# Optimization experiments

Measured on AMD Instinct MI355X. Metric: run time of the kernel, lower is better.

Reference implementation:

```python
import jax, jax.numpy as jnp
import numpy as np

C = 8           # feat_channel
B, N = 8, 64    # batch, max objects
H, W = 128, 128
D = (C + 2) * C + C + C * C + C + C + 1  # 169


def setup_inputs() -> dict:
    key = jax.random.key(0)
    k1, k2, k3, k4 = jax.random.split(key, 4)
    seg_feat = jax.random.normal(k1, (B, C, H, W), dtype=jnp.float32)
    conv_weight = jax.random.normal(k2, (B, D, H, W), dtype=jnp.float32)
    mask = jnp.ones((B, N), dtype=jnp.float32)
    ind = jax.random.randint(k3, (B, N), 0, H * W, dtype=jnp.int64)
    target = jax.random.uniform(k4, (B, N, H, W), dtype=jnp.float32)
    return {"seg_feat": seg_feat, "conv_weight": conv_weight, "mask": mask,
            "ind": ind, "target": target}


def reference(seg_feat, conv_weight, mask, ind, target):
    b, c, h, w = seg_feat.shape
    n = ind.shape[1]
    # _tranpose_and_gather_feat: [B,D,H,W] -> [B,HW,D] -> gather at ind -> [B,N,D]
    wflat = conv_weight.reshape(b, -1, h * w).transpose(0, 2, 1)
    weight = jnp.take_along_axis(wflat, ind[:, :, None], axis=1)  # [B,N,D]
    splits = np.cumsum([(c + 2) * c, c, c * c, c, c])
    w1, b1, w2, b2, w3, b3 = jnp.split(weight, splits, axis=-1)
    w1 = w1.reshape(b, n, c, c + 2)   # per-object conv1 1x1 weights
    w2 = w2.reshape(b, n, c, c)
    w3 = w3.reshape(b, n, 1, c)
    # object centers and relative coordinate maps
    x0 = (ind % w).astype(jnp.float32)
    y0 = (ind // w).astype(jnp.float32)
    xg = jnp.arange(w, dtype=jnp.float32)
    yg = jnp.arange(h, dtype=jnp.float32)
    y_grid, x_grid = jnp.meshgrid(yg, xg, indexing="ij")  # [H,W]
    x_rel = (x_grid[None, None] - x0[:, :, None, None]) / 128.0  # [B,N,H,W]
    y_rel = (y_grid[None, None] - y0[:, :, None, None]) / 128.0
    feat = jnp.concatenate(
        [jnp.broadcast_to(seg_feat[:, None], (b, n, c, h, w)),
         x_rel[:, :, None], y_rel[:, :, None]], axis=2)  # [B,N,C+2,H,W]
    # three grouped 1x1 convs == per-object channel contractions
    h1 = jax.nn.relu(jnp.einsum("bnoc,bnchw->bnohw", w1, feat) + b1[..., None, None])
    h2 = jax.nn.relu(jnp.einsum("bnoc,bnchw->bnohw", w2, h1) + b2[..., None, None])
    out = jax.nn.sigmoid(jnp.einsum("bnoc,bnchw->bnohw", w3, h2) + b3[..., None, None])[:, :, 0]  # [B,N,H,W]
    m = mask[:, :, None, None]
    pred = out * m
    tgt = target * m
    smooth = 1.0
    inter = jnp.sum(pred * tgt, axis=(1, 2, 3))
    denom = jnp.sum(pred * pred, axis=(1, 2, 3)) + jnp.sum(tgt * tgt, axis=(1, 2, 3))
    loss = 1.0 - (2.0 * inter + smooth) / (denom + smooth)  # per-image dice
    return jnp.mean(loss)  # sum over batch / batch_size
```

## Files before the change

### kernel.cpp

```cpp
#include <hip/hip_runtime.h>

#define Cc 8
#define Hh 128
#define Ww 128
#define Nn 64
#define Bb 8
#define Dd 169
#define HW (Hh * Ww)
#define NP 4
#define NPG 8
#define PXS 1024
#define NSTRIPE (HW / PXS)
#define NBLK (Bb * NPG * NSTRIPE)
#define FRAGW 16
#define FRAG_U32 (256 * 64 * FRAGW)
#define SLOTS (NPG * NSTRIPE)

#define INV128 (1.0f / 128.0f)

typedef __fp16 f16x2 __attribute__((ext_vector_type(2)));
typedef _Float16 h8 __attribute__((ext_vector_type(8)));
typedef float f32x4 __attribute__((ext_vector_type(4)));

static __device__ __forceinline__ uint32_t pku(float a, float b) {
    f16x2 t = __builtin_amdgcn_cvt_pkrtz(a, b);
    uint32_t u; __builtin_memcpy(&u, &t, 4); return u;
}
static __device__ __forceinline__ h8 u4h8(uint32_t a, uint32_t b, uint32_t c, uint32_t d) {
    uint32_t u[4] = {a, b, c, d}; h8 r; __builtin_memcpy(&r, u, 16); return r;
}

__global__ void pack_frags(const float* __restrict__ conv_weight,
                           const float* __restrict__ mask,
                           const int*   __restrict__ ind,
                           uint32_t*    __restrict__ frag) {
    const int npair = blockIdx.x;
    const int b     = npair >> 5;
    const int bn0   = b * Nn + 2 * (npair & 31);
    const int l  = threadIdx.x;
    const int g  = l >> 4, r = l & 15, rr = r & 7;
    const int bnr = bn0 + (r >> 3);
    const int bng = bn0 + (g >> 1);
    const float* base = conv_weight + (size_t)b * Dd * HW;
    const float* srcR = base + ind[bnr];
    const float* srcG = base + ind[bng];

    float a1[8];
    #pragma unroll
    for (int e = 0; e < 8; ++e) {
        const int k = 8 * g + e;
        float v = 0.f;
        if (k < 8)       v = srcR[(size_t)(rr * 10 + k) * HW];
        else if (k == 8) v = srcR[(size_t)(rr * 10 + 8) * HW];
        else if (k == 9) v = srcR[(size_t)(rr * 10 + 9) * HW];
        else if (k == 10) {
            const float w8 = srcR[(size_t)(rr * 10 + 8) * HW];
            const float w9 = srcR[(size_t)(rr * 10 + 9) * HW];
            const float b1 = srcR[(size_t)(80 + rr) * HW];
            const int   ib = ind[bnr];
            v = b1 - w8 * ((float)(ib & 127) * INV128)
                   - w9 * ((float)(ib >> 7) * INV128);
        }
        a1[e] = v;
    }
    float a2[4];
    #pragma unroll
    for (int e = 0; e < 4; ++e) {
        const int k2 = 4 * g + e;
        float v = 0.f;
        if (r < 8)  { if (k2 < 8)  v = srcR[(size_t)(88 + rr * 8 + k2) * HW]; }
        else        { if (k2 >= 8) v = srcR[(size_t)(88 + rr * 8 + (k2 - 8)) * HW]; }
        a2[e] = v;
    }
    const float b2bias = (g == 0) ? srcR[(size_t)(152 + rr) * HW] : 0.f;

    float w3v[4];
    #pragma unroll
    for (int j = 0; j < 4; ++j) {
        const int c = (4 * g + j) & 7;
        w3v[j] = srcG[(size_t)(160 + c) * HW];
    }
    const float b3 = srcG[(size_t)168 * HW];
    const float mm = mask[bng];

    uint32_t* dst = frag + ((size_t)npair * 64 + l) * FRAGW;
    dst[0] = pku(a1[0], a1[1]); dst[1] = pku(a1[2], a1[3]);
    dst[2] = pku(a1[4], a1[5]); dst[3] = pku(a1[6], a1[7]);
    dst[4] = pku(a2[0], a2[1]); dst[5] = pku(a2[2], a2[3]);
    dst[6] = pku(b2bias, 0.f);
    float* df = (float*)dst;
    df[7] = w3v[0]; df[8] = w3v[1]; df[9] = w3v[2]; df[10] = w3v[3];
    df[11] = b3; df[12] = mm * mm;
    dst[13] = 0u; dst[14] = 0u; dst[15] = 0u;
}

__global__ __launch_bounds__(256)
__attribute__((amdgpu_waves_per_eu(4)))
void seg_dice_main(const float* __restrict__ seg_feat,
                   const float* __restrict__ target,
                   const uint32_t* __restrict__ frag,
                   float* __restrict__ red_base) {
    const int bid    = blockIdx.x;
    const int b      = bid & 7;
    const int rest   = bid >> 3;
    const int npg    = rest & 7;
    const int stripe = rest >> 3;
    const int p0     = stripe * PXS;
    const int tid  = threadIdx.x;
    const int wave = tid >> 6;
    const int l    = tid & 63;
    const int g    = l >> 4, col = l & 15;

    __shared__ uint4 lds4[PXS];

    const float* seg_b = seg_feat + (size_t)b * Cc * HW;
    #pragma unroll
    for (int q = 0; q < 4; ++q) {
        const int px = q * 256 + tid;
        float v[8];
        #pragma unroll
        for (int c = 0; c < 8; ++c) v[c] = seg_b[(size_t)c * HW + p0 + px];
        lds4[px] = uint4{pku(v[0], v[1]), pku(v[2], v[3]),
                         pku(v[4], v[5]), pku(v[6], v[7])};
    }

    const int npair0 = b * 32 + npg * NP;
    const int par = g & 1;
    uint32_t A1u[NP][4], A2u[NP][3];
    float w3v[NP][4];
    float flS[2], b3S[2];
    const float* ptrS[2];
    #pragma unroll
    for (int j = 0; j < NP; ++j) {
        const uint4* fp = (const uint4*)(frag + ((size_t)(npair0 + j) * 64 + l) * FRAGW);
        const uint4 q0 = fp[0], q1 = fp[1], q2 = fp[2];
        const uint32_t q3x = ((const uint32_t*)fp)[12];
        A1u[j][0] = q0.x; A1u[j][1] = q0.y; A1u[j][2] = q0.z; A1u[j][3] = q0.w;
        A2u[j][0] = q1.x; A2u[j][1] = q1.y; A2u[j][2] = q1.z;
        w3v[j][0] = __uint_as_float(q1.w);
        w3v[j][1] = __uint_as_float(q2.x);
        w3v[j][2] = __uint_as_float(q2.y);
        w3v[j][3] = __uint_as_float(q2.z);
        const int s = j >> 1;
        if ((j & 1) == par) {
            b3S[s] = __uint_as_float(q2.w);
            flS[s] = __uint_as_float(q3x);
            const int bnS = b * Nn + 2 * (npg * NP + j) + (l >> 5);
            ptrS[s] = target + (size_t)bnS * HW + p0 + col;
        }
    }
    __syncthreads();

    const uint32_t one16 = 0x3C00u;
    const uint32_t b2one = (g == 0) ? one16 : 0u;
    const f32x4 ZF = {0.f, 0.f, 0.f, 0.f};
    float inter = 0.f, ps = 0.f, ts = 0.f;

    #pragma unroll 1
    for (int tt = wave; tt < PXS / 16; tt += 4) {
        const int pxt = tt * 16;
        const int pxg = p0 + pxt + col;

        const uint4 d = lds4[pxt + col];
        const uint32_t xv = pku((float)(pxg & 127) * INV128,
                                (float)(pxg >> 7) * INV128);
        const uint32_t e0 = (g == 0) ? d.x : ((g == 1) ? xv : 0u);
        const uint32_t e1 = (g == 0) ? d.y : ((g == 1) ? one16 : 0u);
        const uint32_t e2 = (g == 0) ? d.z : 0u;
        const uint32_t e3 = (g == 0) ? d.w : 0u;
        const h8 B1 = u4h8(e0, e1, e2, e3);

        #pragma unroll
        for (int s = 0; s < 2; ++s) {
            const int jA = 2 * s, jB = 2 * s + 1;
            const h8 A1a = u4h8(A1u[jA][0], A1u[jA][1], A1u[jA][2], A1u[jA][3]);
            const h8 A1b = u4h8(A1u[jB][0], A1u[jB][1], A1u[jB][2], A1u[jB][3]);
            f32x4 h1a = __builtin_amdgcn_mfma_f32_16x16x32_f16(A1a, B1, ZF, 0, 0, 0);
            f32x4 h1b = __builtin_amdgcn_mfma_f32_16x16x32_f16(A1b, B1, ZF, 0, 0, 0);
            #pragma unroll
            for (int e = 0; e < 4; ++e) {
                h1a[e] = fmaxf(h1a[e], 0.f);
                h1b[e] = fmaxf(h1b[e], 0.f);
            }
            const h8 B2a = u4h8(pku(h1a[0], h1a[1]), pku(h1a[2], h1a[3]), b2one, 0u);
            const h8 B2b = u4h8(pku(h1b[0], h1b[1]), pku(h1b[2], h1b[3]), b2one, 0u);
            const h8 A2a = u4h8(A2u[jA][0], A2u[jA][1], A2u[jA][2], 0u);
            const h8 A2b = u4h8(A2u[jB][0], A2u[jB][1], A2u[jB][2], 0u);
            f32x4 h2a = __builtin_amdgcn_mfma_f32_16x16x32_f16(A2a, B2a, ZF, 0, 0, 0);
            f32x4 h2b = __builtin_amdgcn_mfma_f32_16x16x32_f16(A2b, B2b, ZF, 0, 0, 0);

            float zpa = fmaxf(h2a[0], 0.f) * w3v[jA][0];
            zpa = fmaf(fmaxf(h2a[1], 0.f), w3v[jA][1], zpa);
            zpa = fmaf(fmaxf(h2a[2], 0.f), w3v[jA][2], zpa);
            zpa = fmaf(fmaxf(h2a[3], 0.f), w3v[jA][3], zpa);
            float zpb = fmaxf(h2b[0], 0.f) * w3v[jB][0];
            zpb = fmaf(fmaxf(h2b[1], 0.f), w3v[jB][1], zpb);
            zpb = fmaf(fmaxf(h2b[2], 0.f), w3v[jB][2], zpb);
            zpb = fmaf(fmaxf(h2b[3], 0.f), w3v[jB][3], zpb);
            zpa += __shfl_xor(zpa, 16);
            zpb += __shfl_xor(zpb, 16);

            const float z  = (par ? zpb : zpa) + b3S[s];
            const float o  = __builtin_amdgcn_rcpf(1.f + __expf(-z));
            const float tv = ptrS[s][pxt];
            const float fo = flS[s] * o;
            inter = fmaf(fo, tv, inter);
            ps    = fmaf(fo, o, ps);
            ts    = fmaf(flS[s], tv * tv, ts);
        }
    }

    #pragma unroll
    for (int off = 32; off > 0; off >>= 1) {
        inter += __shfl_down(inter, off);
        ps    += __shfl_down(ps,    off);
        ts    += __shfl_down(ts,    off);
    }
    __shared__ float red[3][4];
    if ((tid & 63) == 0) { red[0][wave] = inter; red[1][wave] = ps; red[2][wave] = ts; }
    __syncthreads();
    if (tid == 0) {
        red_base[(b * 3 + 0) * SLOTS + rest] = red[0][0] + red[0][1] + red[0][2] + red[0][3];
        red_base[(b * 3 + 1) * SLOTS + rest] = red[1][0] + red[1][1] + red[1][2] + red[1][3];
        red_base[(b * 3 + 2) * SLOTS + rest] = red[2][0] + red[2][1] + red[2][2] + red[2][3];
    }
}

__global__ void seg_dice_final(const float* __restrict__ red_base, float* __restrict__ out) {
    __shared__ float red[24][4];
    const int tid = threadIdx.x;
    if (tid < 96) {
        const int series = tid >> 2;
        const int part   = tid & 3;
        const float4* p = (const float4*)(red_base + series * SLOTS + part * 32);
        float s = 0.f;
        #pragma unroll
        for (int i = 0; i < 8; ++i) { const float4 v = p[i]; s += (v.x + v.y) + (v.z + v.w); }
        red[series][part] = s;
    }
    __syncthreads();
    if (tid == 0) {
        float acc = 0.f;
        #pragma unroll
        for (int b = 0; b < Bb; ++b) {
            const float inter = red[b*3+0][0] + red[b*3+0][1] + red[b*3+0][2] + red[b*3+0][3];
            const float p2    = red[b*3+1][0] + red[b*3+1][1] + red[b*3+1][2] + red[b*3+1][3];
            const float t2    = red[b*3+2][0] + red[b*3+2][1] + red[b*3+2][2] + red[b*3+2][3];
            acc += 1.0f - (2.0f * inter + 1.0f) / (p2 + t2 + 1.0f);
        }
        out[0] = acc * (1.0f / (float)Bb);
    }
}

extern "C" void kernel_launch(void* const* d_in, const int* in_sizes, int n_in,
                              void* d_out, int out_size, void* d_ws, size_t ws_size,
                              hipStream_t stream) {
    const float* seg_feat    = (const float*)d_in[0];
    const float* conv_weight = (const float*)d_in[1];
    const float* mask        = (const float*)d_in[2];
    const int*   ind         = (const int*)d_in[3];
    const float* target      = (const float*)d_in[4];
    float* out = (float*)d_out;

    uint32_t* fragtab  = (uint32_t*)d_ws;
    float*    red_base = (float*)d_ws + FRAG_U32;

    pack_frags<<<256, 64, 0, stream>>>(conv_weight, mask, ind, fragtab);
    seg_dice_main<<<NBLK, 256, 0, stream>>>(seg_feat, target, fragtab, red_base);
    seg_dice_final<<<1, 128, 0, stream>>>(red_base, out);
}
```

Baseline: 36.05 us.

## Halve object pairs per block, double block count, raise occupancy target

Each block now handles 2 object pairs instead of 4, so the grid doubles from 1024 to 2048 blocks and the waves-per-EU hint rises from 4 to 8. The A fragments are packed into half8 vectors once before the loop, and the target load is moved to the start of each iteration. The aim is more latency hiding through occupancy and earlier issue of the global load. The cost is that each block reloads and converts the seg_feat stripe into LDS for half as much work, and the final reduction has twice as many partial slots to read.

```diff
diff --git a/kernel.cpp b/kernel.cpp
--- a/kernel.cpp
+++ b/kernel.cpp
@@ -7,8 +7,8 @@
 #define Bb 8
 #define Dd 169
 #define HW (Hh * Ww)
-#define NP 4
-#define NPG 8
+#define NP 2
+#define NPG 16
 #define PXS 1024
 #define NSTRIPE (HW / PXS)
 #define NBLK (Bb * NPG * NSTRIPE)
@@ -95,7 +95,7 @@
 }
 
 __global__ __launch_bounds__(256)
-__attribute__((amdgpu_waves_per_eu(4)))
+__attribute__((amdgpu_waves_per_eu(8)))
 void seg_dice_main(const float* __restrict__ seg_feat,
                    const float* __restrict__ target,
                    const uint32_t* __restrict__ frag,
@@ -103,8 +103,8 @@
     const int bid    = blockIdx.x;
     const int b      = bid & 7;
     const int rest   = bid >> 3;
-    const int npg    = rest & 7;
-    const int stripe = rest >> 3;
+    const int npg    = rest & 15;
+    const int stripe = rest >> 4;
     const int p0     = stripe * PXS;
     const int tid  = threadIdx.x;
     const int wave = tid >> 6;
@@ -126,27 +126,26 @@
 
     const int npair0 = b * 32 + npg * NP;
     const int par = g & 1;
-    uint32_t A1u[NP][4], A2u[NP][3];
+    h8 A1h[NP], A2h[NP];
     float w3v[NP][4];
-    float flS[2], b3S[2];
-    const float* ptrS[2];
+    float flS = 0.f, b3S = 0.f;
+    const float* ptrS = target;
     #pragma unroll
     for (int j = 0; j < NP; ++j) {
         const uint4* fp = (const uint4*)(frag + ((size_t)(npair0 + j) * 64 + l) * FRAGW);
         const uint4 q0 = fp[0], q1 = fp[1], q2 = fp[2];
         const uint32_t q3x = ((const uint32_t*)fp)[12];
-        A1u[j][0] = q0.x; A1u[j][1] = q0.y; A1u[j][2] = q0.z; A1u[j][3] = q0.w;
-        A2u[j][0] = q1.x; A2u[j][1] = q1.y; A2u[j][2] = q1.z;
+        A1h[j] = u4h8(q0.x, q0.y, q0.z, q0.w);
+        A2h[j] = u4h8(q1.x, q1.y, q1.z, 0u);
         w3v[j][0] = __uint_as_float(q1.w);
         w3v[j][1] = __uint_as_float(q2.x);
         w3v[j][2] = __uint_as_float(q2.y);
         w3v[j][3] = __uint_as_float(q2.z);
-        const int s = j >> 1;
-        if ((j & 1) == par) {
-            b3S[s] = __uint_as_float(q2.w);
-            flS[s] = __uint_as_float(q3x);
+        if (j == par) {
+            b3S = __uint_as_float(q2.w);
+            flS = __uint_as_float(q3x);
             const int bnS = b * Nn + 2 * (npg * NP + j) + (l >> 5);
-            ptrS[s] = target + (size_t)bnS * HW + p0 + col;
+            ptrS = target + (size_t)bnS * HW + p0 + col;
         }
     }
     __syncthreads();
@@ -160,6 +159,8 @@
     for (int tt = wave; tt < PXS / 16; tt += 4) {
         const int pxt = tt * 16;
         const int pxg = p0 + pxt + col;
+
+        const float tv = ptrS[pxt];
 
         const uint4 d = lds4[pxt + col];
         const uint32_t xv = pku((float)(pxg & 127) * INV128,
@@ -170,44 +171,35 @@
         const uint32_t e3 = (g == 0) ? d.w : 0u;
         const h8 B1 = u4h8(e0, e1, e2, e3);
 
-        #pragma unroll
-        for (int s = 0; s < 2; ++s) {
-            const int jA = 2 * s, jB = 2 * s + 1;
-            const h8 A1a = u4h8(A1u[jA][0], A1u[jA][1], A1u[jA][2], A1u[jA][3]);
-            const h8 A1b = u4h8(A1u[jB][0], A1u[jB][1], A1u[jB][2], A1u[jB][3]);
-            f32x4 h1a = __builtin_amdgcn_mfma_f32_16x16x32_f16(A1a, B1, ZF, 0, 0, 0);
-            f32x4 h1b = __builtin_amdgcn_mfma_f32_16x16x32_f16(A1b, B1, ZF, 0, 0, 0);
-            #pragma unroll
-            for (int e = 0; e < 4; ++e) {
-                h1a[e] = fmaxf(h1a[e], 0.f);
-                h1b[e] = fmaxf(h1b[e], 0.f);
-            }
-            const h8 B2a = u4h8(pku(h1a[0], h1a[1]), pku(h1a[2], h1a[3]), b2one, 0u);
-            const h8 B2b = u4h8(pku(h1b[0], h1b[1]), pku(h1b[2], h1b[3]), b2one, 0u);
-            const h8 A2a = u4h8(A2u[jA][0], A2u[jA][1], A2u[jA][2], 0u);
-            const h8 A2b = u4h8(A2u[jB][0], A2u[jB][1], A2u[jB][2], 0u);
-            f32x4 h2a = __builtin_amdgcn_mfma_f32_16x16x32_f16(A2a, B2a, ZF, 0, 0, 0);
-            f32x4 h2b = __builtin_amdgcn_mfma_f32_16x16x32_f16(A2b, B2b, ZF, 0, 0, 0);
-
-            float zpa = fmaxf(h2a[0], 0.f) * w3v[jA][0];
-            zpa = fmaf(fmaxf(h2a[1], 0.f), w3v[jA][1], zpa);
-            zpa = fmaf(fmaxf(h2a[2], 0.f), w3v[jA][2], zpa);
-            zpa = fmaf(fmaxf(h2a[3], 0.f), w3v[jA][3], zpa);
-            float zpb = fmaxf(h2b[0], 0.f) * w3v[jB][0];
-            zpb = fmaf(fmaxf(h2b[1], 0.f), w3v[jB][1], zpb);
-            zpb = fmaf(fmaxf(h2b[2], 0.f), w3v[jB][2], zpb);
-            zpb = fmaf(fmaxf(h2b[3], 0.f), w3v[jB][3], zpb);
-            zpa += __shfl_xor(zpa, 16);
-            zpb += __shfl_xor(zpb, 16);
-
-            const float z  = (par ? zpb : zpa) + b3S[s];
-            const float o  = __builtin_amdgcn_rcpf(1.f + __expf(-z));
-            const float tv = ptrS[s][pxt];
-            const float fo = flS[s] * o;
-            inter = fmaf(fo, tv, inter);
-            ps    = fmaf(fo, o, ps);
-            ts    = fmaf(flS[s], tv * tv, ts);
-        }
+        f32x4 h1a = __builtin_amdgcn_mfma_f32_16x16x32_f16(A1h[0], B1, ZF, 0, 0, 0);
+        f32x4 h1b = __builtin_amdgcn_mfma_f32_16x16x32_f16(A1h[1], B1, ZF, 0, 0, 0);
+        #pragma unroll
+        for (int e = 0; e < 4; ++e) {
+            h1a[e] = fmaxf(h1a[e], 0.f);
+            h1b[e] = fmaxf(h1b[e], 0.f);
+        }
+        const h8 B2a = u4h8(pku(h1a[0], h1a[1]), pku(h1a[2], h1a[3]), b2one, 0u);
+        const h8 B2b = u4h8(pku(h1b[0], h1b[1]), pku(h1b[2], h1b[3]), b2one, 0u);
+        f32x4 h2a = __builtin_amdgcn_mfma_f32_16x16x32_f16(A2h[0], B2a, ZF, 0, 0, 0);
+        f32x4 h2b = __builtin_amdgcn_mfma_f32_16x16x32_f16(A2h[1], B2b, ZF, 0, 0, 0);
+
+        float zpa = fmaxf(h2a[0], 0.f) * w3v[0][0];
+        zpa = fmaf(fmaxf(h2a[1], 0.f), w3v[0][1], zpa);
+        zpa = fmaf(fmaxf(h2a[2], 0.f), w3v[0][2], zpa);
+        zpa = fmaf(fmaxf(h2a[3], 0.f), w3v[0][3], zpa);
+        float zpb = fmaxf(h2b[0], 0.f) * w3v[1][0];
+        zpb = fmaf(fmaxf(h2b[1], 0.f), w3v[1][1], zpb);
+        zpb = fmaf(fmaxf(h2b[2], 0.f), w3v[1][2], zpb);
+        zpb = fmaf(fmaxf(h2b[3], 0.f), w3v[1][3], zpb);
+        zpa += __shfl_xor(zpa, 16);
+        zpb += __shfl_xor(zpb, 16);
+
+        const float z  = (par ? zpb : zpa) + b3S;
+        const float o  = __builtin_amdgcn_rcpf(1.f + __expf(-z));
+        const float fo = flS * o;
+        inter = fmaf(fo, tv, inter);
+        ps    = fmaf(fo, o, ps);
+        ts    = fmaf(flS, tv * tv, ts);
     }
 
     #pragma unroll
@@ -232,10 +224,10 @@
     if (tid < 96) {
         const int series = tid >> 2;
         const int part   = tid & 3;
-        const float4* p = (const float4*)(red_base + series * SLOTS + part * 32);
+        const float4* p = (const float4*)(red_base + series * SLOTS + part * 64);
         float s = 0.f;
         #pragma unroll
-        for (int i = 0; i < 8; ++i) { const float4 v = p[i]; s += (v.x + v.y) + (v.z + v.w); }
+        for (int i = 0; i < 16; ++i) { const float4 v = p[i]; s += (v.x + v.y) + (v.z + v.w); }
         red[series][part] = s;
     }
     __syncthreads();
```

Result: no change. 36.14 us (+0.2%).
